# Performance work log

Hardware: AMD Instinct MI355X
Metric: run time of the kernel (lower is better)

## Reference

```python
import jax, jax.numpy as jnp
import numpy as np

N, E = 50000, 800000
IN_FEATS, H, L = 16, 64, 3


def _glorot(key, shape):
    fan_in = shape[-1]
    return jax.random.normal(key, shape, dtype=jnp.float32) / np.sqrt(fan_in)


def setup_inputs() -> dict:
    key = jax.random.key(0)
    ks = jax.random.split(key, 12)
    return {
        "features": jax.random.normal(ks[0], (N, IN_FEATS), dtype=jnp.float32),
        "src": jax.random.randint(ks[1], (E,), 0, N, dtype=jnp.int32),
        "dst": jax.random.randint(ks[2], (E,), 0, N, dtype=jnp.int32),
        # input_module: Linear(in_feats, hidden)
        "W_in": _glorot(ks[3], (IN_FEATS, H)),
        "b_in": jnp.zeros((H,), jnp.float32),
        # edge_module: Linear(2*hidden, 1), shared across layers
        "W_edge": _glorot(ks[4], (2 * H, 1)),
        "b_edge": jnp.zeros((1,), jnp.float32),
        # per-layer GRUCell params (torch layout: [3H, H] for W_ih/W_hh)
        "Wih": _glorot(ks[5], (L, 3 * H, H)),
        "Whh": _glorot(ks[6], (L, 3 * H, H)),
        "bih": jnp.zeros((L, 3 * H), jnp.float32),
        "bhh": jnp.zeros((L, 3 * H), jnp.float32),
        # edge_predictor: Linear(2*hidden, 1)
        "W_pred": _glorot(ks[7], (2 * H, 1)),
        "b_pred": jnp.zeros((1,), jnp.float32),
    }


def _gru_cell(x, h, W_ih, W_hh, b_ih, b_hh):
    # torch.nn.GRUCell math
    gi = x @ W_ih.T + b_ih  # [N, 3H]
    gh = h @ W_hh.T + b_hh  # [N, 3H]
    i_r, i_z, i_n = jnp.split(gi, 3, axis=1)
    h_r, h_z, h_n = jnp.split(gh, 3, axis=1)
    r = jax.nn.sigmoid(i_r + h_r)
    z = jax.nn.sigmoid(i_z + h_z)
    n = jnp.tanh(i_n + r * h_n)
    return (1.0 - z) * n + z * h


def reference(features, src, dst, W_in, b_in, W_edge, b_edge, Wih, Whh, bih, bhh, W_pred, b_pred):
    n_nodes = features.shape[0]
    h = features @ W_in + b_in  # [N, H]
    num_layers = Wih.shape[0]
    for l in range(num_layers):
        h_u = h[src]  # [E, H] gather src
        h_v = h[dst]  # [E, H] gather dst
        # shared edge module: sigmoid(Linear(cat[h_u, h_v]))
        w = jax.nn.sigmoid(jnp.concatenate([h_u, h_v], axis=1) @ W_edge + b_edge)  # [E, 1]
        m = h_u * w  # messages [E, H]
        h_new = jax.ops.segment_sum(m, dst, num_segments=n_nodes)  # scatter-sum to dst
        h = _gru_cell(h_new, h, Wih[l], Whh[l], bih[l], bhh[l])
    edges_h = jnp.concatenate([h[src], h[dst]], axis=1)  # [E, 2H]
    return (edges_h @ W_pred + b_pred).squeeze()  # [E]
```

## Files before the change

kernel.cpp:

```cpp
#include <hip/hip_runtime.h>
#include <hip/hip_bf16.h>

#define H 64
#define H3 192
#define ITEMS 16

typedef __attribute__((ext_vector_type(8))) short short8;
typedef __attribute__((ext_vector_type(4))) float f32x4;

__device__ __forceinline__ float sigmoidf_(float x) {
    return 1.0f / (1.0f + __expf(-x));
}
__device__ __forceinline__ float tanhf_(float x) {
    float e = __expf(2.0f * x);
    return 1.0f - 2.0f / (e + 1.0f);
}
__device__ __forceinline__ unsigned short f2bf(float f) {
    unsigned u = __builtin_bit_cast(unsigned, f);
    u += 0x7FFFu + ((u >> 16) & 1u);
    return (unsigned short)(u >> 16);
}
__device__ __forceinline__ float bf2f(unsigned short s) {
    return __builtin_bit_cast(float, (unsigned)s << 16);
}

__global__ __launch_bounds__(256) void setup_kernel(
    const float* __restrict__ feat, const float* __restrict__ Win,
    const float* __restrict__ bin, const float* __restrict__ Wg,
    float* __restrict__ h, unsigned short* __restrict__ h_bf,
    float* __restrict__ a_gate, float* __restrict__ b_gate,
    const float* __restrict__ Wih, const float* __restrict__ Whh,
    unsigned short* __restrict__ w_bf,
    const int* __restrict__ dst, int* __restrict__ bhist,
    int N, int E, int per, int nbA, int nbB, int nb_c)
{
    int bid = blockIdx.x;
    int t = threadIdx.x;
    if (bid < nbA) {
        __shared__ float sWin[16 * H];
        __shared__ float sbin[H];
        __shared__ float sWg[2 * H];
        for (int i = t; i < 16 * H; i += 256) sWin[i] = Win[i];
        if (t < H) sbin[t] = bin[t];
        if (t < 2 * H) sWg[t] = Wg[t];
        __syncthreads();

        int n = bid * 256 + t;
        if (n >= N) return;

        float f[16];
        const float4* fr = (const float4*)(feat + (size_t)n * 16);
#pragma unroll
        for (int i = 0; i < 4; i++) {
            float4 v = fr[i];
            f[4 * i + 0] = v.x; f[4 * i + 1] = v.y;
            f[4 * i + 2] = v.z; f[4 * i + 3] = v.w;
        }
        float a = 0.f, b = 0.f;
        float* hrow = h + (size_t)n * H;
        unsigned short* brow = h_bf + (size_t)n * H;
        for (int j = 0; j < H; j++) {
            float hj = sbin[j];
#pragma unroll
            for (int k = 0; k < 16; k++) hj += f[k] * sWin[k * H + j];
            hrow[j] = hj;
            brow[j] = f2bf(hj);
            a += hj * sWg[j];
            b += hj * sWg[H + j];
        }
        a_gate[n] = a;
        b_gate[n] = b;
    } else if (bid < nbA + nbB) {
        int i = (bid - nbA) * 256 + t;
        if (i < per) w_bf[i] = f2bf(Wih[i]);
        else if (i < 2 * per) w_bf[i] = f2bf(Whh[i - per]);
    } else {
        __shared__ int lh[256];
        lh[t] = 0;
        __syncthreads();
        int base = (bid - nbA - nbB) * (256 * ITEMS);
#pragma unroll
        for (int k = 0; k < ITEMS; k++) {
            int i = base + k * 256 + t;
            if (i < E) atomicAdd(&lh[dst[i] >> 8], 1);
        }
        __syncthreads();
        bhist[t * nb_c + (bid - nbA - nbB)] = lh[t];
    }
}

__global__ __launch_bounds__(256) void scan_pass1(
    const int* __restrict__ deg, int* __restrict__ locals,
    int* __restrict__ bsum, int N)
{
    int t = threadIdx.x;
    int i = blockIdx.x * 256 + t;
    int v = (i < N) ? deg[i] : 0;
    int lane = t & 63, w = t >> 6;
    int s = v;
#pragma unroll
    for (int off = 1; off < 64; off <<= 1) {
        int u = __shfl_up(s, off);
        if (lane >= off) s += u;
    }
    __shared__ int wsum[4];
    if (lane == 63) wsum[w] = s;
    __syncthreads();
    int add = 0;
    for (int k = 0; k < w; k++) add += wsum[k];
    if (i < N) locals[i] = s + add - v;
    if (t == 255) bsum[blockIdx.x] = s + add;
}

__global__ __launch_bounds__(256) void scan_pass3c(
    const int* __restrict__ locals, const int* __restrict__ bsum,
    int* __restrict__ S, int M, int E, int mb)
{
    int t = threadIdx.x;
    int b = blockIdx.x;
    int v = 0;
    for (int k = t; k < b && k < mb; k += 256) v += bsum[k];
#pragma unroll
    for (int off = 32; off >= 1; off >>= 1) v += __shfl_xor(v, off);
    __shared__ int ws[4];
    if ((t & 63) == 0) ws[t >> 6] = v;
    __syncthreads();
    int carry = ws[0] + ws[1] + ws[2] + ws[3];

    int i = b * 256 + t;
    if (i < M) S[i] = locals[i] + carry;
    else if (i == M) S[M] = E;
}

__global__ __launch_bounds__(256) void bucket_scatter_kernel(
    const int* __restrict__ src, const int* __restrict__ dst,
    const int* __restrict__ S, unsigned* __restrict__ pk, int E, int nb_c)
{
    __shared__ int lbase[256];
    __shared__ int lrun[256];
    int t = threadIdx.x;
    lbase[t] = S[t * nb_c + blockIdx.x];
    lrun[t] = 0;
    __syncthreads();
    int base = blockIdx.x * (256 * ITEMS);
#pragma unroll
    for (int k = 0; k < ITEMS; k++) {
        int i = base + k * 256 + t;
        if (i < E) {
            int d = dst[i];
            int b = d >> 8;
            int r = atomicAdd(&lrun[b], 1);
            pk[lbase[b] + r] = ((unsigned)(d & 255) << 16) | (unsigned)src[i];
        }
    }
}

__global__ __launch_bounds__(256) void bucket_finalize_kernel(
    const unsigned* __restrict__ pk, const int* __restrict__ S,
    int* __restrict__ offsets, unsigned short* __restrict__ csr16,
    int N, int E, int nb_c, int NB)
{
    __shared__ int lh[256];
    __shared__ int loff[256];
    __shared__ int lrun[256];
    int t = threadIdx.x;
    int b = blockIdx.x;
    int beg = S[b * nb_c];
    int endb = (b + 1 < NB) ? S[(b + 1) * nb_c] : E;
    lh[t] = 0; lrun[t] = 0;
    __syncthreads();
    for (int i = beg + t; i < endb; i += 256) atomicAdd(&lh[pk[i] >> 16], 1);
    __syncthreads();
    int v = lh[t];
    loff[t] = v;
    __syncthreads();
    for (int off = 1; off < 256; off <<= 1) {
        int u = (t >= off) ? loff[t - off] : 0;
        __syncthreads();
        loff[t] += u;
        __syncthreads();
    }
    int excl = loff[t] - v;
    int node = b * 256 + t;
    if (node < N) offsets[node] = beg + excl;
    if (b == NB - 1 && t == 0) offsets[N] = E;
    loff[t] = excl;
    __syncthreads();
    for (int i = beg + t; i < endb; i += 256) {
        unsigned w = pk[i];
        int d = (int)(w >> 16);
        int r = atomicAdd(&lrun[d], 1);
        csr16[beg + loff[d] + r] = (unsigned short)(w & 0xFFFFu);
    }
}

__global__ __launch_bounds__(256) void aggregate_kernel(
    const unsigned short* __restrict__ h_bf, const float* __restrict__ a_gate,
    const float* __restrict__ b_gate, const int* __restrict__ offsets,
    const unsigned short* __restrict__ csr16, const float* __restrict__ b_edge,
    unsigned short* __restrict__ hnew_bf, int N)
{
    int wid = threadIdx.x >> 6;
    int lane = threadIdx.x & 63;
    int sub = lane >> 3;
    int cg  = lane & 7;
    int v = blockIdx.x * 4 + wid;
    if (v >= N) return;

    int beg = offsets[v];
    int end = offsets[v + 1];
    float bv = b_gate[v] + b_edge[0];
    float acc0[8] = {0.f, 0.f, 0.f, 0.f, 0.f, 0.f, 0.f, 0.f};
    float acc1[8] = {0.f, 0.f, 0.f, 0.f, 0.f, 0.f, 0.f, 0.f};

    for (int cs = beg; cs < end; cs += 64) {
        int m = end - cs; if (m > 64) m = 64;
        int u = 0; float w = 0.f;
        if (lane < m) {
            u = (int)csr16[cs + lane];
            w = sigmoidf_(a_gate[u] + bv);
        }
        for (int j = 0; j < m; j += 16) {
            int e0 = j + sub, e1 = j + 8 + sub;
            int u0 = __shfl(u, e0 & 63);
            float w0 = __shfl(w, e0 & 63);
            int u1 = __shfl(u, e1 & 63);
            float w1 = __shfl(w, e1 & 63);
            if (e0 >= m) w0 = 0.f;
            if (e1 >= m) w1 = 0.f;
            short8 hv0 = *(const short8*)(h_bf + (size_t)u0 * H + cg * 8);
            short8 hv1 = *(const short8*)(h_bf + (size_t)u1 * H + cg * 8);
#pragma unroll
            for (int k = 0; k < 8; k++)
                acc0[k] += w0 * bf2f((unsigned short)hv0[k]);
#pragma unroll
            for (int k = 0; k < 8; k++)
                acc1[k] += w1 * bf2f((unsigned short)hv1[k]);
        }
    }
#pragma unroll
    for (int k = 0; k < 8; k++) acc0[k] += acc1[k];
#pragma unroll
    for (int mm = 8; mm < 64; mm <<= 1) {
#pragma unroll
        for (int k = 0; k < 8; k++)
            acc0[k] += __shfl_xor(acc0[k], mm);
    }
    if (sub == 0) {
        short8 o;
#pragma unroll
        for (int k = 0; k < 8; k++) o[k] = (short)f2bf(acc0[k]);
        *(short8*)(hnew_bf + (size_t)v * H + cg * 8) = o;
    }
}

__global__ __launch_bounds__(256) void gru_mfma_kernel(
    const unsigned short* __restrict__ x_bf,
    float* __restrict__ h,
    unsigned short* __restrict__ h_bf,
    const unsigned short* __restrict__ wih_bf,
    const unsigned short* __restrict__ whh_bf,
    const float* __restrict__ bih, const float* __restrict__ bhh,
    const float* __restrict__ Wg,
    float* __restrict__ a_gate, float* __restrict__ b_gate, int N)
{
    int lane = threadIdx.x & 63;
    int wv = threadIdx.x >> 6;
    int c = lane & 15;
    int g = lane >> 4;
    int nbase = blockIdx.x * 64 + wv * 16;
    if (nbase >= N) return;

    int nrow = nbase + c;
    int nclamp = nrow < N ? nrow : (N - 1);

    short8 ax[2], ah[2];
#pragma unroll
    for (int ch = 0; ch < 2; ch++) {
        ax[ch] = *(const short8*)(x_bf + (size_t)nclamp * H + ch * 32 + g * 8);
        ah[ch] = *(const short8*)(h_bf + (size_t)nclamp * H + ch * 32 + g * 8);
    }

    f32x4 gi[12], gh[12];
#pragma unroll
    for (int jb = 0; jb < 12; jb++) {
        gi[jb] = (f32x4){0.f, 0.f, 0.f, 0.f};
        gh[jb] = (f32x4){0.f, 0.f, 0.f, 0.f};
    }

#pragma unroll
    for (int jb = 0; jb < 12; jb++) {
        const unsigned short* wi = wih_bf + (size_t)(jb * 16 + c) * H + g * 8;
        const unsigned short* wh = whh_bf + (size_t)(jb * 16 + c) * H + g * 8;
        short8 wi0 = *(const short8*)(wi);
        short8 wi1 = *(const short8*)(wi + 32);
        short8 wh0 = *(const short8*)(wh);
        short8 wh1 = *(const short8*)(wh + 32);
        gi[jb] = __builtin_amdgcn_mfma_f32_16x16x32_bf16(ax[0], wi0, gi[jb], 0, 0, 0);
        gi[jb] = __builtin_amdgcn_mfma_f32_16x16x32_bf16(ax[1], wi1, gi[jb], 0, 0, 0);
        gh[jb] = __builtin_amdgcn_mfma_f32_16x16x32_bf16(ah[0], wh0, gh[jb], 0, 0, 0);
        gh[jb] = __builtin_amdgcn_mfma_f32_16x16x32_bf16(ah[1], wh1, gh[jb], 0, 0, 0);
    }

    float pa[4] = {0.f, 0.f, 0.f, 0.f};
    float pb[4] = {0.f, 0.f, 0.f, 0.f};
#pragma unroll
    for (int jb = 0; jb < 4; jb++) {
        int j = jb * 16 + c;
        float br = bih[j] + bhh[j];
        float bz = bih[H + j] + bhh[H + j];
        float bin_ = bih[2 * H + j];
        float bhn_ = bhh[2 * H + j];
        float wga = Wg[j], wgb = Wg[H + j];
#pragma unroll
        for (int q = 0; q < 4; q++) {
            int node = nbase + g * 4 + q;
            float r = sigmoidf_(gi[jb][q] + gh[jb][q] + br);
            float z = sigmoidf_(gi[jb + 4][q] + gh[jb + 4][q] + bz);
            float nn = tanhf_(gi[jb + 8][q] + bin_ + r * (gh[jb + 8][q] + bhn_));
            size_t idx = (size_t)node * H + j;
            float hp = h[idx];
            float ho = (1.0f - z) * nn + z * hp;
            h[idx] = ho;
            h_bf[idx] = f2bf(ho);
            pa[q] += ho * wga;
            pb[q] += ho * wgb;
        }
    }
#pragma unroll
    for (int m = 1; m < 16; m <<= 1) {
#pragma unroll
        for (int q = 0; q < 4; q++) {
            pa[q] += __shfl_xor(pa[q], m);
            pb[q] += __shfl_xor(pb[q], m);
        }
    }
    if (c == 0) {
#pragma unroll
        for (int q = 0; q < 4; q++) {
            int node = nbase + g * 4 + q;
            a_gate[node] = pa[q];
            b_gate[node] = pb[q];
        }
    }
}

__global__ __launch_bounds__(256) void predict_kernel(
    const int* __restrict__ src, const int* __restrict__ dst,
    const float* __restrict__ pa, const float* __restrict__ pb,
    const float* __restrict__ b_pred, float* __restrict__ out, int E)
{
    int e4 = (blockIdx.x * 256 + threadIdx.x) * 4;
    float bp = b_pred[0];
    if (e4 + 3 < E) {
        int4 s = *(const int4*)(src + e4);
        int4 d = *(const int4*)(dst + e4);
        float4 o;
        o.x = pa[s.x] + pb[d.x] + bp;
        o.y = pa[s.y] + pb[d.y] + bp;
        o.z = pa[s.z] + pb[d.z] + bp;
        o.w = pa[s.w] + pb[d.w] + bp;
        *(float4*)(out + e4) = o;
    } else {
        for (int e = e4; e < E; e++)
            out[e] = pa[src[e]] + pb[dst[e]] + bp;
    }
}

extern "C" void kernel_launch(void* const* d_in, const int* in_sizes, int n_in,
                              void* d_out, int out_size, void* d_ws, size_t ws_size,
                              hipStream_t stream) {
    const float* features = (const float*)d_in[0];
    const int*   src      = (const int*)d_in[1];
    const int*   dst      = (const int*)d_in[2];
    const float* W_in     = (const float*)d_in[3];
    const float* b_in     = (const float*)d_in[4];
    const float* W_edge   = (const float*)d_in[5];
    const float* b_edge   = (const float*)d_in[6];
    const float* Wih      = (const float*)d_in[7];
    const float* Whh      = (const float*)d_in[8];
    const float* bih      = (const float*)d_in[9];
    const float* bhh      = (const float*)d_in[10];
    const float* W_pred   = (const float*)d_in[11];
    const float* b_pred   = (const float*)d_in[12];
    float* out = (float*)d_out;

    int N = in_sizes[0] / 16;
    int E = in_sizes[1];
    int L = in_sizes[7] / (H3 * H);
    int per = L * H3 * H;

    int nb_nodes = (N + 255) / 256;
    int nb_agg   = (N + 3) / 4;
    int nb_gru   = (N + 63) / 64;
    int nb_conv  = (2 * per + 255) / 256;
    int nb_pred  = (E + 1023) / 1024;

    int nb_c = (E + 256 * ITEMS - 1) / (256 * ITEMS);
    int NB   = (N + 255) / 256;
    int M    = 256 * nb_c;
    int mb   = (M + 255) / 256;
    int nb_s3 = (M + 1 + 255) / 256;

    float* h = (float*)d_ws;
    unsigned short* h_bf = (unsigned short*)(h + (size_t)N * H);
    unsigned short* hnew_bf = h_bf + (size_t)N * H;
    unsigned short* w_bf = hnew_bf + (size_t)N * H;
    float* a_gate = (float*)(w_bf + 2 * per);
    float* b_gate = a_gate + N;
    int* offsets  = (int*)(b_gate + N);
    unsigned* pk  = (unsigned*)(offsets + N + 1);
    unsigned short* csr16 = (unsigned short*)(pk + E);
    int* bhist = (int*)(csr16 + E);
    int* bloc  = bhist + M;
    int* sbh   = bloc + M;
    int* bsum  = sbh + M + 1;

    setup_kernel<<<nb_nodes + nb_conv + nb_c, 256, 0, stream>>>(
        features, W_in, b_in, W_edge, h, h_bf, a_gate, b_gate,
        Wih, Whh, w_bf, dst, bhist,
        N, E, per, nb_nodes, nb_conv, nb_c);

    scan_pass1<<<mb, 256, 0, stream>>>(bhist, bloc, bsum, M);
    scan_pass3c<<<nb_s3, 256, 0, stream>>>(bloc, bsum, sbh, M, E, mb);
    bucket_scatter_kernel<<<nb_c, 256, 0, stream>>>(src, dst, sbh, pk, E, nb_c);
    bucket_finalize_kernel<<<NB, 256, 0, stream>>>(pk, sbh, offsets, csr16, N, E, nb_c, NB);

    for (int l = 0; l < L; l++) {
        aggregate_kernel<<<nb_agg, 256, 0, stream>>>(
            h_bf, a_gate, b_gate, offsets, csr16, b_edge, hnew_bf, N);
        const float* Wg = (l < L - 1) ? W_edge : W_pred;
        gru_mfma_kernel<<<nb_gru, 256, 0, stream>>>(
            hnew_bf, h, h_bf,
            w_bf + (size_t)l * H3 * H,
            w_bf + (size_t)per + (size_t)l * H3 * H,
            bih + (size_t)l * H3, bhh + (size_t)l * H3,
            Wg, a_gate, b_gate, N);
    }

    predict_kernel<<<nb_pred, 256, 0, stream>>>(src, dst, a_gate, b_gate, b_pred, out, E);
}
```

Measured before the change: 247.1 us.

## Drop fp32 hidden state in favor of bf16 and fuse two-pass scan

Removes the fp32 copy of the node hidden state: setup and the GRU kernel now read the previous hidden value from the bf16 buffer and write only bf16, which cuts HBM traffic per layer. The two scan kernels are also merged into one, where each block sums all earlier histogram entries directly and then does its local scan, saving a launch and intermediate buffers. The cost is that the recurrent state now carries bf16 rounding across layers, which loosens accuracy, and each scan block does redundant prefix reads that grow with its block index.

```diff
diff --git a/kernel.cpp b/kernel.cpp
--- a/kernel.cpp
+++ b/kernel.cpp
@@ -27,7 +27,7 @@
 __global__ __launch_bounds__(256) void setup_kernel(
     const float* __restrict__ feat, const float* __restrict__ Win,
     const float* __restrict__ bin, const float* __restrict__ Wg,
-    float* __restrict__ h, unsigned short* __restrict__ h_bf,
+    unsigned short* __restrict__ h_bf,
     float* __restrict__ a_gate, float* __restrict__ b_gate,
     const float* __restrict__ Wih, const float* __restrict__ Whh,
     unsigned short* __restrict__ w_bf,
@@ -57,13 +57,11 @@
             f[4 * i + 2] = v.z; f[4 * i + 3] = v.w;
         }
         float a = 0.f, b = 0.f;
-        float* hrow = h + (size_t)n * H;
         unsigned short* brow = h_bf + (size_t)n * H;
         for (int j = 0; j < H; j++) {
             float hj = sbin[j];
 #pragma unroll
             for (int k = 0; k < 16; k++) hj += f[k] * sWin[k * H + j];
-            hrow[j] = hj;
             brow[j] = f2bf(hj);
             a += hj * sWg[j];
             b += hj * sWg[H + j];
@@ -89,15 +87,26 @@
     }
 }
 
-__global__ __launch_bounds__(256) void scan_pass1(
-    const int* __restrict__ deg, int* __restrict__ locals,
-    int* __restrict__ bsum, int N)
+__global__ __launch_bounds__(256) void scan_fused(
+    const int* __restrict__ bhist, int* __restrict__ S, int M, int E)
 {
     int t = threadIdx.x;
-    int i = blockIdx.x * 256 + t;
-    int v = (i < N) ? deg[i] : 0;
+    int b = blockIdx.x;
+    int pre = b * 256;
+    if (pre > M) pre = M;
+    int v = 0;
+    for (int k = t; k < pre; k += 256) v += bhist[k];
+#pragma unroll
+    for (int off = 32; off >= 1; off >>= 1) v += __shfl_xor(v, off);
+    __shared__ int ws[4];
+    if ((t & 63) == 0) ws[t >> 6] = v;
+    __syncthreads();
+    int carry = ws[0] + ws[1] + ws[2] + ws[3];
+
+    int i = b * 256 + t;
+    int x = (i < M) ? bhist[i] : 0;
     int lane = t & 63, w = t >> 6;
-    int s = v;
+    int s = x;
 #pragma unroll
     for (int off = 1; off < 64; off <<= 1) {
         int u = __shfl_up(s, off);
@@ -108,27 +117,7 @@
     __syncthreads();
     int add = 0;
     for (int k = 0; k < w; k++) add += wsum[k];
-    if (i < N) locals[i] = s + add - v;
-    if (t == 255) bsum[blockIdx.x] = s + add;
-}
-
-__global__ __launch_bounds__(256) void scan_pass3c(
-    const int* __restrict__ locals, const int* __restrict__ bsum,
-    int* __restrict__ S, int M, int E, int mb)
-{
-    int t = threadIdx.x;
-    int b = blockIdx.x;
-    int v = 0;
-    for (int k = t; k < b && k < mb; k += 256) v += bsum[k];
-#pragma unroll
-    for (int off = 32; off >= 1; off >>= 1) v += __shfl_xor(v, off);
-    __shared__ int ws[4];
-    if ((t & 63) == 0) ws[t >> 6] = v;
-    __syncthreads();
-    int carry = ws[0] + ws[1] + ws[2] + ws[3];
-
-    int i = b * 256 + t;
-    if (i < M) S[i] = locals[i] + carry;
+    if (i < M) S[i] = carry + s + add - x;
     else if (i == M) S[M] = E;
 }
 
@@ -256,7 +245,6 @@
 
 __global__ __launch_bounds__(256) void gru_mfma_kernel(
     const unsigned short* __restrict__ x_bf,
-    float* __restrict__ h,
     unsigned short* __restrict__ h_bf,
     const unsigned short* __restrict__ wih_bf,
     const unsigned short* __restrict__ whh_bf,
@@ -319,9 +307,8 @@
             float z = sigmoidf_(gi[jb + 4][q] + gh[jb + 4][q] + bz);
             float nn = tanhf_(gi[jb + 8][q] + bin_ + r * (gh[jb + 8][q] + bhn_));
             size_t idx = (size_t)node * H + j;
-            float hp = h[idx];
+            float hp = bf2f(h_bf[idx]);
             float ho = (1.0f - z) * nn + z * hp;
-            h[idx] = ho;
             h_bf[idx] = f2bf(ho);
             pa[q] += ho * wga;
             pb[q] += ho * wgb;
@@ -399,11 +386,9 @@
     int nb_c = (E + 256 * ITEMS - 1) / (256 * ITEMS);
     int NB   = (N + 255) / 256;
     int M    = 256 * nb_c;
-    int mb   = (M + 255) / 256;
-    int nb_s3 = (M + 1 + 255) / 256;
-
-    float* h = (float*)d_ws;
-    unsigned short* h_bf = (unsigned short*)(h + (size_t)N * H);
+    int nb_scan = (M + 1 + 255) / 256;
+
+    unsigned short* h_bf = (unsigned short*)d_ws;
     unsigned short* hnew_bf = h_bf + (size_t)N * H;
     unsigned short* w_bf = hnew_bf + (size_t)N * H;
     float* a_gate = (float*)(w_bf + 2 * per);
@@ -412,17 +397,14 @@
     unsigned* pk  = (unsigned*)(offsets + N + 1);
     unsigned short* csr16 = (unsigned short*)(pk + E);
     int* bhist = (int*)(csr16 + E);
-    int* bloc  = bhist + M;
-    int* sbh   = bloc + M;
-    int* bsum  = sbh + M + 1;
+    int* sbh   = bhist + M;
 
     setup_kernel<<<nb_nodes + nb_conv + nb_c, 256, 0, stream>>>(
-        features, W_in, b_in, W_edge, h, h_bf, a_gate, b_gate,
+        features, W_in, b_in, W_edge, h_bf, a_gate, b_gate,
         Wih, Whh, w_bf, dst, bhist,
         N, E, per, nb_nodes, nb_conv, nb_c);
 
-    scan_pass1<<<mb, 256, 0, stream>>>(bhist, bloc, bsum, M);
-    scan_pass3c<<<nb_s3, 256, 0, stream>>>(bloc, bsum, sbh, M, E, mb);
+    scan_fused<<<nb_scan, 256, 0, stream>>>(bhist, sbh, M, E);
     bucket_scatter_kernel<<<nb_c, 256, 0, stream>>>(src, dst, sbh, pk, E, nb_c);
     bucket_finalize_kernel<<<NB, 256, 0, stream>>>(pk, sbh, offsets, csr16, N, E, nb_c, NB);
 
@@ -431,7 +413,7 @@
             h_bf, a_gate, b_gate, offsets, csr16, b_edge, hnew_bf, N);
         const float* Wg = (l < L - 1) ? W_edge : W_pred;
         gru_mfma_kernel<<<nb_gru, 256, 0, stream>>>(
-            hnew_bf, h, h_bf,
+            hnew_bf, h_bf,
             w_bf + (size_t)l * H3 * H,
             w_bf + (size_t)per + (size_t)l * H3 * H,
             bih + (size_t)l * H3, bhh + (size_t)l * H3,
```

New measurement: 256.1 us. 3.6% more time.
